# Performance work log

Measured on AMD Instinct MI355X. Metric: run time of the kernel, lower is better.

## Reference

```python
import jax, jax.numpy as jnp
import numpy as np

BETA = 1e-8
ALPHA = 0.5
CHOOSE_K = 128
MEMORY_SIZE = 65536
KEY_DIM = 256
BATCH = 1024


def _l2norm(x, axis=-1, eps=1e-12):
    return x / jnp.sqrt(jnp.sum(x * x, axis=axis, keepdims=True) + eps)


def setup_inputs() -> dict:
    key = jax.random.key(0)
    k1, k2, k3 = jax.random.split(key, 3)
    q = _l2norm(jax.random.normal(k1, (BATCH, KEY_DIM), dtype=jnp.float32))
    memory_key = _l2norm(jax.random.normal(k2, (MEMORY_SIZE, KEY_DIM), dtype=jnp.float32))
    # module init: hist[:] = 1e-5; add small random variation so topk is non-degenerate
    memory_hist = 1e-5 + 1e-3 * jax.random.uniform(k3, (MEMORY_SIZE,), dtype=jnp.float32)
    # module init: values = ones, second half zeroed
    memory_values = jnp.concatenate([
        jnp.ones((MEMORY_SIZE // 2,), dtype=jnp.float32),
        jnp.zeros((MEMORY_SIZE - MEMORY_SIZE // 2,), dtype=jnp.float32),
    ])
    return {"q": q, "memory_key": memory_key,
            "memory_hist": memory_hist, "memory_values": memory_values}


def reference(q, memory_key, memory_hist, memory_values):
    # obtain_topk over FULL memory: dense similarity [B, M]
    sims = jnp.matmul(q, memory_key.T)                      # [B, M]
    scores = jnp.exp(sims - 1.0) * (memory_hist + BETA)[None, :]
    _, k_idxs = jax.lax.top_k(scores, CHOOSE_K)             # [B, K]

    # gather reduced memory at topk indices
    red_keys = memory_key[k_idxs]                           # [B, K, D]
    red_hist = memory_hist[k_idxs] * ALPHA                  # [B, K]
    red_vals = memory_values[k_idxs]                        # [B, K]

    # posterior over the K gathered slots
    sim_k = jnp.einsum('bd,bkd->bk', q, red_keys)           # [B, K]
    joint = jnp.exp(sim_k - 1.0) * (red_hist + BETA)        # [B, K]
    posterior = joint / jnp.sum(joint, axis=1, keepdims=True)
    result = jnp.sum(posterior * red_vals, axis=1)          # [B]
    return result
```

## Files before the change

kernel.cpp:

```cpp
#include <hip/hip_runtime.h>

#define BATCH   1024
#define MSIZE   65536
#define KDIM    256
#define CHOOSEK 128
#define SELK    160
#define BETA    1e-8f
#define ALPHA   0.5f
#define KSCALE  426666.7f

typedef short bf16x8 __attribute__((ext_vector_type(8)));
typedef float f32x4  __attribute__((ext_vector_type(4)));

__device__ inline unsigned int pack2bf(float a, float b) {
    unsigned int ua = __float_as_uint(a);
    unsigned int ub = __float_as_uint(b);
    ua += 0x7fffu + ((ua >> 16) & 1u);
    ub += 0x7fffu + ((ub >> 16) & 1u);
    return (ua >> 16) | (ub & 0xffff0000u);
}

#define GLD16(g, l) __builtin_amdgcn_global_load_lds( \
    (const __attribute__((address_space(1))) unsigned int*)(g), \
    (__attribute__((address_space(3))) unsigned int*)(l), 16, 0, 0)

__global__ __launch_bounds__(256)
void convert_kernel(const float* __restrict__ q, const float* __restrict__ key,
                    unsigned short* __restrict__ qb, unsigned short* __restrict__ kb)
{
    const int id = blockIdx.x * 256 + threadIdx.x;
    const float* src; unsigned short* dst; int off;
    if (blockIdx.x < 128) { src = q;   dst = qb; off = id; }
    else                  { src = key; dst = kb; off = id - 32768; }
    const float4* s4 = (const float4*)src;
    float4 a = s4[off * 2];
    float4 b = s4[off * 2 + 1];
    uint4 p = make_uint4(pack2bf(a.x, a.y), pack2bf(a.z, a.w),
                         pack2bf(b.x, b.y), pack2bf(b.z, b.w));
    ((uint4*)dst)[off] = p;
}

__global__ __launch_bounds__(256)
void score_kernel(const unsigned short* __restrict__ qb,
                  const unsigned short* __restrict__ kb,
                  const float* __restrict__ hist,
                  unsigned char* __restrict__ s8)
{
    __shared__ __align__(16) unsigned short As[4][128 * 32];
    __shared__ __align__(16) unsigned short Bs[4][128 * 32];
    const int tid = threadIdx.x;
    const int bid = blockIdx.x;
    const int b0 = ((bid >> 3) & 7) * 128;
    const int n0 = ((bid & 7) + ((bid >> 6) << 3)) * 128;
    const int lane = tid & 63, wave = tid >> 6;
    const int wm = (wave >> 1) * 64, wn = (wave & 1) * 64;
    const int l15 = lane & 15, l4 = lane >> 4;

    f32x4 acc[4][4] = {};

    const int srow = tid >> 2;
    const int seg  = (tid & 3) * 8;
    const unsigned short* gA = qb + (size_t)(b0 + srow) * KDIM + seg;
    const unsigned short* gB = kb + (size_t)(n0 + srow) * KDIM + seg;
    const int lofs = srow * 32 + seg;

#define STAGE(st) do {                                             \
    const int _ko = (st) * 32;                                     \
    GLD16(gA + _ko,             &As[(st) & 3][lofs]);              \
    GLD16(gA + _ko + 64 * KDIM, &As[(st) & 3][lofs + 64 * 32]);    \
    GLD16(gB + _ko,             &Bs[(st) & 3][lofs]);              \
    GLD16(gB + _ko + 64 * KDIM, &Bs[(st) & 3][lofs + 64 * 32]);    \
} while (0)

#define STEP(s, WN) do {                                                     \
    asm volatile("s_waitcnt vmcnt(" #WN ")" ::: "memory");                   \
    __builtin_amdgcn_s_barrier();                                            \
    asm volatile("" ::: "memory");                                           \
    if ((s) + 3 < 8) STAGE((s) + 3);                                         \
    bf16x8 qf[4], kf[4];                                                     \
    _Pragma("unroll")                                                        \
    for (int j = 0; j < 4; ++j)                                              \
        qf[j] = *(const bf16x8*)(&As[(s) & 3][(wm + j * 16 + l15) * 32 + l4 * 8]); \
    _Pragma("unroll")                                                        \
    for (int i = 0; i < 4; ++i)                                              \
        kf[i] = *(const bf16x8*)(&Bs[(s) & 3][(wn + i * 16 + l15) * 32 + l4 * 8]); \
    _Pragma("unroll")                                                        \
    for (int i = 0; i < 4; ++i)                                              \
        _Pragma("unroll")                                                    \
        for (int j = 0; j < 4; ++j)                                          \
            acc[i][j] = __builtin_amdgcn_mfma_f32_16x16x32_bf16(kf[i], qf[j], acc[i][j], 0, 0, 0); \
} while (0)

    STAGE(0); STAGE(1); STAGE(2);

    STEP(0, 8); STEP(1, 8); STEP(2, 8); STEP(3, 8);
    STEP(4, 8); STEP(5, 8); STEP(6, 4); STEP(7, 0);

#undef STEP
#undef STAGE

    float4 hj[4];
#pragma unroll
    for (int i = 0; i < 4; ++i) {
        float4 h = *(const float4*)&hist[n0 + wn + i * 16 + l4 * 4];
        hj[i] = make_float4((h.x + BETA) * KSCALE, (h.y + BETA) * KSCALE,
                            (h.z + BETA) * KSCALE, (h.w + BETA) * KSCALE);
    }
#pragma unroll
    for (int j = 0; j < 4; ++j) {
        const size_t row = (size_t)(b0 + wm + j * 16 + l15) * MSIZE;
#pragma unroll
        for (int i = 0; i < 4; ++i) {
            const float* hv = (const float*)&hj[i];
            unsigned int pk = 0;
#pragma unroll
            for (int reg = 0; reg < 4; ++reg) {
                float sc = __expf(acc[i][j][reg] - 1.0f) * hv[reg];
                pk |= (unsigned int)(unsigned char)(int)fminf(sc, 255.0f) << (8 * reg);
            }
            *(unsigned int*)(s8 + row + (n0 + wn + i * 16 + l4 * 4)) = pk;
        }
    }
}

__global__ __launch_bounds__(256, 4)
void select_kernel(const float* __restrict__ q,
                   const float* __restrict__ key,
                   const float* __restrict__ hist,
                   const float* __restrict__ vals,
                   const unsigned char* __restrict__ s8,
                   float* __restrict__ out)
{
    const int b   = blockIdx.x;
    const int tid = threadIdx.x;

    __shared__ __align__(16) float qs[KDIM];
    __shared__ unsigned int hcnt[16 * 257];
    __shared__ int   stot[256];
    __shared__ int   scal[2];
    __shared__ int   cidx[1024];
    __shared__ float csc[1024], cjj[1024], cjv[1024];
    __shared__ float wred[8];

    qs[tid] = q[(size_t)b * KDIM + tid];
    const uint4* rowp = reinterpret_cast<const uint4*>(s8 + (size_t)b * MSIZE);
    const int rep = (tid & 15) * 257;

    int H = -1;
    int minb = 128;
    for (;;) {
        for (int i = tid; i < 16 * 257; i += 256) hcnt[i] = 0u;
        if (tid == 0) { scal[0] = -1; scal[1] = 0; }
        __syncthreads();

        for (int i = 0; i < 16; ++i) {
            uint4 v = rowp[i * 256 + tid];
            unsigned int w[4] = {v.x, v.y, v.z, v.w};
#pragma unroll
            for (int k = 0; k < 4; ++k) {
                if (minb == 0 || (w[k] & 0x80808080u)) {
#pragma unroll
                    for (int jj = 0; jj < 4; ++jj) {
                        int bb = (int)((w[k] >> (8 * jj)) & 0xffu);
                        if (bb >= minb) atomicAdd(&hcnt[rep + bb], 1u);
                    }
                }
            }
        }
        __syncthreads();
        { unsigned int t = 0;
#pragma unroll
          for (int k = 0; k < 16; ++k) t += hcnt[k * 257 + tid];
          stot[tid] = (int)t; }
        __syncthreads();

        if (tid < 64) {
            const int l = tid;
            int t0 = stot[l * 4], t1 = stot[l * 4 + 1], t2 = stot[l * 4 + 2], t3 = stot[l * 4 + 3];
            int lsum = t0 + t1 + t2 + t3;
            int s = lsum;
#pragma unroll
            for (int off = 1; off < 64; off <<= 1) {
                int u = __shfl_down(s, off, 64);
                if (l + off < 64) s += u;
            }
            int A  = s - lsum;
            int S3 = A + t3;
            int S2 = S3 + t2;
            int S1 = S2 + t1;
            int S0 = S1 + t0;
            if (S0 >= SELK && S1 < SELK) scal[0] = l * 4 + 0;
            if (S1 >= SELK && S2 < SELK) scal[0] = l * 4 + 1;
            if (S2 >= SELK && S3 < SELK) scal[0] = l * 4 + 2;
            if (S3 >= SELK && A  < SELK) scal[0] = l * 4 + 3;
        }
        __syncthreads();
        H = scal[0];
        __syncthreads();
        if (H >= 0) break;
        minb = 0;
    }

    const unsigned int uH = (unsigned int)H;
    const bool pre = (H >= 128);
    for (int i = 0; i < 16; ++i) {
        uint4 v = rowp[i * 256 + tid];
        const int base = (i * 256 + tid) * 16;
        unsigned int w[4] = {v.x, v.y, v.z, v.w};
#pragma unroll
        for (int k = 0; k < 4; ++k) {
            if (!pre || (w[k] & 0x80808080u)) {
#pragma unroll
                for (int jj = 0; jj < 4; ++jj) {
                    unsigned int bb = (w[k] >> (8 * jj)) & 0xffu;
                    if (bb >= uH) {
                        int p = atomicAdd(&scal[1], 1);
                        if (p < 1024) cidx[p] = base + 4 * k + jj;
                    }
                }
            }
        }
    }
    __syncthreads();
    const int ncand = min(scal[1], 1024);

    const int gid = tid >> 4, gl = tid & 15;
    const float4* q4 = (const float4*)qs;
    for (int i = gid; i < ncand; i += 16) {
        const int idx = cidx[i];
        const float4* kp = (const float4*)(key + (size_t)idx * KDIM);
        float p = 0.f;
#pragma unroll
        for (int u = 0; u < 4; ++u) {
            float4 kk = kp[gl * 4 + u];
            float4 qq = q4[gl * 4 + u];
            p += kk.x * qq.x + kk.y * qq.y + kk.z * qq.z + kk.w * qq.w;
        }
#pragma unroll
        for (int off = 1; off < 16; off <<= 1) p += __shfl_xor(p, off, 64);
        if (gl == 0) {
            float e = expf(p - 1.0f);
            float h = hist[idx];
            csc[i] = e * (h + BETA);
            float j = e * (ALPHA * h + BETA);
            cjj[i] = j;
            cjv[i] = j * vals[idx];
        }
    }
    __syncthreads();

    const int wave = tid >> 6, lane = tid & 63;
    float pn = 0.f, pd = 0.f;
    for (int i = tid; i < ncand; i += 256) {
        float si = csc[i]; int ii = cidx[i]; int rank = 0;
        for (int t = 0; t < ncand; ++t) {
            float st = csc[t];
            rank += (st > si || (st == si && cidx[t] < ii)) ? 1 : 0;
        }
        if (rank < CHOOSEK) { pn += cjv[i]; pd += cjj[i]; }
    }
#pragma unroll
    for (int off = 32; off > 0; off >>= 1) {
        pn += __shfl_xor(pn, off, 64);
        pd += __shfl_xor(pd, off, 64);
    }
    if (lane == 0) { wred[wave] = pn; wred[4 + wave] = pd; }
    __syncthreads();
    if (tid == 0) {
        float n = wred[0] + wred[1] + wred[2] + wred[3];
        float d = wred[4] + wred[5] + wred[6] + wred[7];
        out[b] = n / d;
    }
}

extern "C" void kernel_launch(void* const* d_in, const int* in_sizes, int n_in,
                              void* d_out, int out_size, void* d_ws, size_t ws_size,
                              hipStream_t stream)
{
    (void)in_sizes; (void)n_in; (void)out_size; (void)ws_size;
    const float* q    = (const float*)d_in[0];
    const float* key  = (const float*)d_in[1];
    const float* hist = (const float*)d_in[2];
    const float* vals = (const float*)d_in[3];
    float* out = (float*)d_out;

    unsigned char*  s8 = (unsigned char*)d_ws;
    unsigned short* kb = (unsigned short*)((char*)d_ws + ((size_t)64 << 20));
    unsigned short* qb = (unsigned short*)((char*)d_ws + ((size_t)96 << 20));

    convert_kernel<<<8320, 256, 0, stream>>>(q, key, qb, kb);
    score_kernel<<<4096, 256, 0, stream>>>(qb, kb, hist, s8);
    select_kernel<<<BATCH, 256, 0, stream>>>(q, key, hist, vals, s8, out);
}
```

Measured before the change: 224.1 us.

## Pre-swizzle Q into MFMA fragment layout, quantize scores in log domain

```diff
diff --git a/kernel.cpp b/kernel.cpp
--- a/kernel.cpp
+++ b/kernel.cpp
@@ -7,7 +7,8 @@
 #define SELK    160
 #define BETA    1e-8f
 #define ALPHA   0.5f
-#define KSCALE  426666.7f
+#define KSC  425.0f
+#define KOFF 7.2f
 
 typedef short bf16x8 __attribute__((ext_vector_type(8)));
 typedef float f32x4  __attribute__((ext_vector_type(4)));
@@ -26,28 +27,40 @@
 
 __global__ __launch_bounds__(256)
 void convert_kernel(const float* __restrict__ q, const float* __restrict__ key,
-                    unsigned short* __restrict__ qb, unsigned short* __restrict__ kb)
+                    const float* __restrict__ hist,
+                    unsigned short* __restrict__ qs, unsigned short* __restrict__ kb,
+                    float* __restrict__ Ltab)
 {
-    const int id = blockIdx.x * 256 + threadIdx.x;
-    const float* src; unsigned short* dst; int off;
-    if (blockIdx.x < 128) { src = q;   dst = qb; off = id; }
-    else                  { src = key; dst = kb; off = id - 32768; }
-    const float4* s4 = (const float4*)src;
-    float4 a = s4[off * 2];
-    float4 b = s4[off * 2 + 1];
-    uint4 p = make_uint4(pack2bf(a.x, a.y), pack2bf(a.z, a.w),
-                         pack2bf(b.x, b.y), pack2bf(b.z, b.w));
-    ((uint4*)dst)[off] = p;
-}
-
-__global__ __launch_bounds__(256)
-void score_kernel(const unsigned short* __restrict__ qb,
+    const int bid = blockIdx.x, tid = threadIdx.x;
+    if (bid < 8192) {
+        const int off = bid * 256 + tid;
+        const float4* s4 = (const float4*)key;
+        float4 a = s4[off * 2], b = s4[off * 2 + 1];
+        ((uint4*)kb)[off] = make_uint4(pack2bf(a.x, a.y), pack2bf(a.z, a.w),
+                                       pack2bf(b.x, b.y), pack2bf(b.z, b.w));
+    } else if (bid < 8320) {
+        const int f = (bid - 8192) * 256 + tid;
+        const int l = f & 63, j = (f >> 6) & 3, ks = (f >> 8) & 7;
+        const int wmg = (f >> 11) & 1, bt = f >> 12;
+        const int r = bt * 128 + wmg * 64 + j * 16 + (l & 15);
+        const int c = ks * 32 + (l >> 4) * 8;
+        const float* src = q + (size_t)r * KDIM + c;
+        float4 a = *(const float4*)src, b = *(const float4*)(src + 4);
+        ((uint4*)qs)[f] = make_uint4(pack2bf(a.x, a.y), pack2bf(a.z, a.w),
+                                     pack2bf(b.x, b.y), pack2bf(b.z, b.w));
+    } else {
+        const int n = (bid - 8320) * 256 + tid;
+        Ltab[n] = (logf(hist[n] + BETA) + KOFF) * KSC;
+    }
+}
+
+__global__ __launch_bounds__(256, 3)
+void score_kernel(const unsigned short* __restrict__ qs,
                   const unsigned short* __restrict__ kb,
-                  const float* __restrict__ hist,
+                  const float* __restrict__ Ltab,
                   unsigned char* __restrict__ s8)
 {
-    __shared__ __align__(16) unsigned short As[4][128 * 32];
-    __shared__ __align__(16) unsigned short Bs[4][128 * 32];
+    __shared__ __align__(16) unsigned short Bs[3][128 * 32];
     const int tid = threadIdx.x;
     const int bid = blockIdx.x;
     const int b0 = ((bid >> 3) & 7) * 128;
@@ -55,35 +68,35 @@
     const int lane = tid & 63, wave = tid >> 6;
     const int wm = (wave >> 1) * 64, wn = (wave & 1) * 64;
     const int l15 = lane & 15, l4 = lane >> 4;
+    const int bt = (bid >> 3) & 7, wmg = wave >> 1;
 
     f32x4 acc[4][4] = {};
 
     const int srow = tid >> 2;
     const int seg  = (tid & 3) * 8;
-    const unsigned short* gA = qb + (size_t)(b0 + srow) * KDIM + seg;
     const unsigned short* gB = kb + (size_t)(n0 + srow) * KDIM + seg;
     const int lofs = srow * 32 + seg;
 
-#define STAGE(st) do {                                             \
-    const int _ko = (st) * 32;                                     \
-    GLD16(gA + _ko,             &As[(st) & 3][lofs]);              \
-    GLD16(gA + _ko + 64 * KDIM, &As[(st) & 3][lofs + 64 * 32]);    \
-    GLD16(gB + _ko,             &Bs[(st) & 3][lofs]);              \
-    GLD16(gB + _ko + 64 * KDIM, &Bs[(st) & 3][lofs + 64 * 32]);    \
+    const bf16x8* qw = (const bf16x8*)qs + ((bt * 2 + wmg) * 8) * 4 * 64 + lane;
+
+#define STAGE_B(st) do {                                             \
+    const int _ko = (st) * 32;                                       \
+    GLD16(gB + _ko,             &Bs[(st) % 3][lofs]);                \
+    GLD16(gB + _ko + 64 * KDIM, &Bs[(st) % 3][lofs + 64 * 32]);     \
 } while (0)
 
 #define STEP(s, WN) do {                                                     \
     asm volatile("s_waitcnt vmcnt(" #WN ")" ::: "memory");                   \
     __builtin_amdgcn_s_barrier();                                            \
     asm volatile("" ::: "memory");                                           \
-    if ((s) + 3 < 8) STAGE((s) + 3);                                         \
-    bf16x8 qf[4], kf[4];                                                     \
+    bf16x8 qf[4];                                                            \
     _Pragma("unroll")                                                        \
-    for (int j = 0; j < 4; ++j)                                              \
-        qf[j] = *(const bf16x8*)(&As[(s) & 3][(wm + j * 16 + l15) * 32 + l4 * 8]); \
+    for (int j = 0; j < 4; ++j) qf[j] = qw[(((s) * 4 + j) * 64)];            \
+    if ((s) + 2 < 8) STAGE_B((s) + 2);                                       \
+    bf16x8 kf[4];                                                            \
     _Pragma("unroll")                                                        \
     for (int i = 0; i < 4; ++i)                                              \
-        kf[i] = *(const bf16x8*)(&Bs[(s) & 3][(wn + i * 16 + l15) * 32 + l4 * 8]); \
+        kf[i] = *(const bf16x8*)(&Bs[(s) % 3][(wn + i * 16 + l15) * 32 + l4 * 8]); \
     _Pragma("unroll")                                                        \
     for (int i = 0; i < 4; ++i)                                              \
         _Pragma("unroll")                                                    \
@@ -91,32 +104,30 @@
             acc[i][j] = __builtin_amdgcn_mfma_f32_16x16x32_bf16(kf[i], qf[j], acc[i][j], 0, 0, 0); \
 } while (0)
 
-    STAGE(0); STAGE(1); STAGE(2);
-
-    STEP(0, 8); STEP(1, 8); STEP(2, 8); STEP(3, 8);
-    STEP(4, 8); STEP(5, 8); STEP(6, 4); STEP(7, 0);
+    STAGE_B(0); STAGE_B(1);
+
+    STEP(0, 2); STEP(1, 2); STEP(2, 2); STEP(3, 2);
+    STEP(4, 2); STEP(5, 2); STEP(6, 2); STEP(7, 0);
 
 #undef STEP
-#undef STAGE
-
-    float4 hj[4];
-#pragma unroll
-    for (int i = 0; i < 4; ++i) {
-        float4 h = *(const float4*)&hist[n0 + wn + i * 16 + l4 * 4];
-        hj[i] = make_float4((h.x + BETA) * KSCALE, (h.y + BETA) * KSCALE,
-                            (h.z + BETA) * KSCALE, (h.w + BETA) * KSCALE);
-    }
+#undef STAGE_B
+
+    float4 Lv[4];
+#pragma unroll
+    for (int i = 0; i < 4; ++i)
+        Lv[i] = *(const float4*)&Ltab[n0 + wn + i * 16 + l4 * 4];
 #pragma unroll
     for (int j = 0; j < 4; ++j) {
         const size_t row = (size_t)(b0 + wm + j * 16 + l15) * MSIZE;
 #pragma unroll
         for (int i = 0; i < 4; ++i) {
-            const float* hv = (const float*)&hj[i];
+            const float* lv = (const float*)&Lv[i];
             unsigned int pk = 0;
 #pragma unroll
             for (int reg = 0; reg < 4; ++reg) {
-                float sc = __expf(acc[i][j][reg] - 1.0f) * hv[reg];
-                pk |= (unsigned int)(unsigned char)(int)fminf(sc, 255.0f) << (8 * reg);
+                float x = fmaf(acc[i][j][reg], KSC, lv[reg]);
+                x = fminf(fmaxf(x, 0.0f), 255.0f);
+                pk |= (unsigned int)(int)x << (8 * reg);
             }
             *(unsigned int*)(s8 + row + (n0 + wn + i * 16 + l4 * 4)) = pk;
         }
@@ -286,9 +297,10 @@
 
     unsigned char*  s8 = (unsigned char*)d_ws;
     unsigned short* kb = (unsigned short*)((char*)d_ws + ((size_t)64 << 20));
-    unsigned short* qb = (unsigned short*)((char*)d_ws + ((size_t)96 << 20));
-
-    convert_kernel<<<8320, 256, 0, stream>>>(q, key, qb, kb);
-    score_kernel<<<4096, 256, 0, stream>>>(qb, kb, hist, s8);
+    unsigned short* qsw= (unsigned short*)((char*)d_ws + ((size_t)96 << 20));
+    float*          Lt = (float*)((char*)d_ws + ((size_t)96 << 20) + (512 << 10));
+
+    convert_kernel<<<8576, 256, 0, stream>>>(q, key, hist, qsw, kb, Lt);
+    score_kernel<<<4096, 256, 0, stream>>>(qsw, kb, Lt, s8);
     select_kernel<<<BATCH, 256, 0, stream>>>(q, key, hist, vals, s8, out);
 }
```

Measured after the change: 212.8 us. 5.0% less time.
